# Kernel optimization log

Measured on AMD Instinct MI355X. Metric: run time of the kernel, lower is better.

Reference implementation:

```python
import jax, jax.numpy as jnp
import numpy as np
from jax import lax

B, T, F, H, L = 64, 2048, 128, 128, 2


def _lstm_layer(x, Wih, Whh, bih, bhh, h0, c0):
    """Single LSTM layer, torch gate order (i,f,g,o). x: [B,T,in] -> y: [B,T,H], hT, cT."""
    b = bih + bhh

    def step(carry, xt):
        h, c = carry
        gates = xt @ Wih.T + h @ Whh.T + b  # [B,4H]
        i, f, g, o = jnp.split(gates, 4, axis=-1)
        i = jax.nn.sigmoid(i)
        f = jax.nn.sigmoid(f)
        g = jnp.tanh(g)
        o = jax.nn.sigmoid(o)
        c = f * c + i * g
        h = o * jnp.tanh(c)
        return (h, c), h

    xs = jnp.swapaxes(x, 0, 1)  # [T,B,in]
    (hT, cT), ys = lax.scan(step, (h0, c0), xs)
    return jnp.swapaxes(ys, 0, 1), hT, cT


def setup_inputs() -> dict:
    key = jax.random.key(0)
    ks = jax.random.split(key, 20)
    s = 1.0 / np.sqrt(H)
    u = lambda k, shape: jax.random.uniform(k, shape, jnp.float32, -s, s)
    inp = {"x": jax.random.normal(ks[0], (B, T, F), jnp.float32)}
    i = 1
    for pre, in0 in (("enc", F), ("dec", H)):
        for l in range(L):
            d_in = in0 if l == 0 else H
            inp[f"{pre}_Wih{l}"] = u(ks[i], (4 * H, d_in)); i += 1
            inp[f"{pre}_Whh{l}"] = u(ks[i], (4 * H, H)); i += 1
            inp[f"{pre}_bih{l}"] = u(ks[i], (4 * H,)); i += 1
            inp[f"{pre}_bhh{l}"] = u(ks[i], (4 * H,)); i += 1
    inp["out_W"] = u(ks[i], (F, H)); i += 1
    inp["out_b"] = u(ks[i], (F,))
    return inp


def reference(x,
              enc_Wih0, enc_Whh0, enc_bih0, enc_bhh0,
              enc_Wih1, enc_Whh1, enc_bih1, enc_bhh1,
              dec_Wih0, dec_Whh0, dec_bih0, dec_bhh0,
              dec_Wih1, dec_Whh1, dec_bih1, dec_bhh1,
              out_W, out_b):
    z = jnp.zeros((x.shape[0], H), x.dtype)
    # encoder: 2 stacked layers, zero initial state
    y0, h0, c0 = _lstm_layer(x, enc_Wih0, enc_Whh0, enc_bih0, enc_bhh0, z, z)
    y1, h1, c1 = _lstm_layer(y0, enc_Wih1, enc_Whh1, enc_bih1, enc_bhh1, z, z)
    # decoder: zeros input, initial state = encoder final (h,c) per layer
    dec_in = jnp.zeros_like(x)  # valid since n_features == hidden_dim
    d0, _, _ = _lstm_layer(dec_in, dec_Wih0, dec_Whh0, dec_bih0, dec_bhh0, h0, c0)
    d1, _, _ = _lstm_layer(d0, dec_Wih1, dec_Whh1, dec_bih1, dec_bhh1, h1, c1)
    return d1 @ out_W.T + out_b
```

## Files before the change

### kernel.cpp

```cpp
#include <hip/hip_runtime.h>
#include <cstdint>
#include <cstddef>

typedef float    float4v __attribute__((ext_vector_type(4)));
typedef _Float16 f16x4   __attribute__((ext_vector_type(4)));
typedef _Float16 f16x8   __attribute__((ext_vector_type(8)));
typedef unsigned long long u64;

#define DI __device__ __forceinline__

static const int Bsz = 64, Tlen = 2048, Hd = 128, G4 = 512;
static const int Mrows = Bsz * Tlen;
static const int HSTR = 144;
static const int RING = 256;
static const int YSTR = 136;

DI float sigf_fast(float x) {
    float e = __builtin_amdgcn_exp2f(-1.442695041f * x);
    return __builtin_amdgcn_rcpf(1.f + e);
}
DI float tanhf_fast(float x) {
    float e = __builtin_amdgcn_exp2f(-2.885390082f * x);
    return 2.f * __builtin_amdgcn_rcpf(1.f + e) - 1.f;
}

DI void lds_barrier() {
    asm volatile("s_waitcnt lgkmcnt(0)\n\ts_barrier" ::: "memory");
}

DI void pin(f16x8& v) {
    float4v t = __builtin_bit_cast(float4v, v);
    asm volatile("" : "+v"(t));
    v = __builtin_bit_cast(f16x8, t);
}

DI f16x8 cvt8(const float* p) {
    float4v u = *(const float4v*)p;
    float4v w = *(const float4v*)(p + 4);
    f16x8 o;
    o[0] = (_Float16)u[0]; o[1] = (_Float16)u[1]; o[2] = (_Float16)u[2]; o[3] = (_Float16)u[3];
    o[4] = (_Float16)w[0]; o[5] = (_Float16)w[1]; o[6] = (_Float16)w[2]; o[7] = (_Float16)w[3];
    return o;
}

DI u64 ald64(const void* pp) {
    return __hip_atomic_load((const u64*)pp, __ATOMIC_RELAXED, __HIP_MEMORY_SCOPE_AGENT);
}
DI void ast16(void* pp, unsigned short v) {
    __hip_atomic_store((unsigned short*)pp, v, __ATOMIC_RELAXED, __HIP_MEMORY_SCOPE_AGENT);
}
DI unsigned int aldu32(const unsigned int* pp) {
    return __hip_atomic_load(pp, __ATOMIC_RELAXED, __HIP_MEMORY_SCOPE_AGENT);
}
DI void astu32(unsigned int* pp, unsigned int v) {
    __hip_atomic_store(pp, v, __ATOMIC_RELAXED, __HIP_MEMORY_SCOPE_AGENT);
}

template <bool A_F16, bool PERM, bool OUT_F32>
__global__ __launch_bounds__(256) void gemm_k128(
    const void* __restrict__ Av, const float* __restrict__ W,
    const float* __restrict__ bias, void* __restrict__ Cout, int M, int N)
{
    const int lane = threadIdx.x & 63, wave = threadIdx.x >> 6;
    const int m0 = blockIdx.y * 64 + wave * 16;
    const int n0 = blockIdx.x * 64;
    const int r15 = lane & 15, kg = lane >> 4;

    f16x8 a[4];
    if (A_F16) {
        const f16x8* Ar = (const f16x8*)((const _Float16*)Av + (size_t)(m0 + r15) * 128);
#pragma unroll
        for (int kt = 0; kt < 4; kt++) a[kt] = Ar[kt * 4 + kg];
    } else {
        const float* Ar = (const float*)Av + (size_t)(m0 + r15) * 128;
#pragma unroll
        for (int kt = 0; kt < 4; kt++) a[kt] = cvt8(Ar + kt * 32 + kg * 8);
    }

    f16x8 bfrg[4][4];
#pragma unroll
    for (int nt = 0; nt < 4; nt++) {
        int n = n0 + nt * 16 + r15;
        int wrow = PERM ? ((n & 3) * 128 + (n >> 2)) : n;
        const float* Wr = W + (size_t)wrow * 128;
#pragma unroll
        for (int kt = 0; kt < 4; kt++) bfrg[nt][kt] = cvt8(Wr + kt * 32 + kg * 8);
    }

    float4v acc[4] = {};
#pragma unroll
    for (int kt = 0; kt < 4; kt++)
#pragma unroll
        for (int nt = 0; nt < 4; nt++)
            acc[nt] = __builtin_amdgcn_mfma_f32_16x16x32_f16(a[kt], bfrg[nt][kt], acc[nt], 0, 0, 0);

#pragma unroll
    for (int nt = 0; nt < 4; nt++) {
        int n = n0 + nt * 16 + r15;
        float bv = bias ? bias[n] : 0.f;
#pragma unroll
        for (int r = 0; r < 4; r++) {
            int m = m0 + kg * 4 + r;
            float v = acc[nt][r] + bv;
            if (OUT_F32) ((float*)Cout)[(size_t)m * N + n] = v;
            else         ((_Float16*)Cout)[(size_t)m * N + n] = (_Float16)v;
        }
    }
}

template <bool P_HAS_XP, bool P_INIT, bool C_INIT, bool C_WRITE_Y>
__global__ __launch_bounds__(512, 1) void lstm_fused3(
    const float* __restrict__ Up, const float* __restrict__ bip, const float* __restrict__ bhp,
    const _Float16* __restrict__ XPp,
    const float* __restrict__ php, const float* __restrict__ pcp,
    float* __restrict__ fhp, float* __restrict__ fcp,
    const float* __restrict__ Wc, const float* __restrict__ Uc,
    const float* __restrict__ bic, const float* __restrict__ bhc,
    const float* __restrict__ phc, const float* __restrict__ pcc,
    float* __restrict__ fhc, float* __restrict__ fcc,
    _Float16* __restrict__ PB,
    _Float16* __restrict__ X2,
    _Float16* __restrict__ Yc,
    unsigned int* __restrict__ prog, unsigned int* __restrict__ prog2, int T)
{
    const int tid  = threadIdx.x;
    const int lane = tid & 63, w = tid >> 6;
    const int col  = lane & 15, quad = lane >> 4;
    const int b    = col & 3, s = col >> 2;
    const int role = blockIdx.x >> 4;
    const int p    = blockIdx.x & 15;
    const int bglob = p * 4 + b;
    const int j    = w * 16 + s * 4 + quad;
    const int NG   = T >> 3;

    __shared__ alignas(16) _Float16 Hl[2 * 4 * HSTR];
    __shared__ alignas(16) _Float16 Ylh[32 * YSTR];

    unsigned int* pr  = prog  + p * 16;
    unsigned int* pr2 = prog2 + p * 16;

    if (role == 0) {
        f16x8 af[4][4];
#pragma unroll
        for (int mt = 0; mt < 4; mt++) {
            int urow = (col & 3) * 128 + (w * 16 + mt * 4 + (col >> 2));
            const float* ur = Up + (size_t)urow * 128;
#pragma unroll
            for (int kc = 0; kc < 4; kc++) af[mt][kc] = cvt8(ur + kc * 32 + quad * 8);
        }
#pragma unroll
        for (int mt = 0; mt < 4; mt++)
#pragma unroll
            for (int kc = 0; kc < 4; kc++) pin(af[mt][kc]);

        float bq[4];
#pragma unroll
        for (int q = 0; q < 4; q++) bq[q] = bip[q * 128 + j] + bhp[q * 128 + j];

        float c = 0.f, hv = 0.f;
        if (P_INIT) {
            c  = pcp[(size_t)bglob * 128 + j];
            hv = php[(size_t)bglob * 128 + j];
        }
        Hl[b * HSTR + j] = (_Float16)hv;
        __syncthreads();

        const _Float16* xb = P_HAS_XP ? XPp + ((size_t)bglob * T) * 512 + 4 * j : nullptr;
        unsigned short* pbp = (unsigned short*)PB + (size_t)bglob * RING * 128 + j;
        f16x4 xp = {};
        if (P_HAS_XP) xp = *(const f16x4*)xb;

        int cur = 0;
        for (int g = 0; g < NG; g++) {
#pragma unroll
            for (int k = 0; k < 8; k++) {
                const int t = g * 8 + k;
                f16x4 xpn = {};
                if (P_HAS_XP) xpn = *(const f16x4*)(xb + (size_t)(t + 1) * 512);

                const _Float16* Hc = Hl + cur * (4 * HSTR);
                f16x8 bf[4];
#pragma unroll
                for (int kc = 0; kc < 4; kc++)
                    bf[kc] = *(const f16x8*)(Hc + b * HSTR + kc * 32 + quad * 8);

                float4v acc[4] = {};
#pragma unroll
                for (int kc = 0; kc < 4; kc++)
#pragma unroll
                    for (int mt = 0; mt < 4; mt++)
                        acc[mt] = __builtin_amdgcn_mfma_f32_16x16x32_f16(af[mt][kc], bf[kc], acc[mt], 0, 0, 0);

                float4v t0 = (s & 1) ? acc[1] : acc[0];
                float4v t1 = (s & 1) ? acc[3] : acc[2];
                float4v gg = (s & 2) ? t1 : t0;

                float g0 = gg[0] + bq[0], g1 = gg[1] + bq[1], g2 = gg[2] + bq[2], g3 = gg[3] + bq[3];
                if (P_HAS_XP) { g0 += (float)xp[0]; g1 += (float)xp[1]; g2 += (float)xp[2]; g3 += (float)xp[3]; }
                float iv = sigf_fast(g0), fv = sigf_fast(g1);
                float gv = tanhf_fast(g2), ov = sigf_fast(g3);
                c  = fv * c + iv * gv;
                hv = ov * tanhf_fast(c);

                _Float16 hf = (_Float16)hv;
                Hl[(cur ^ 1) * (4 * HSTR) + b * HSTR + j] = hf;

                ast16(pbp + (size_t)(t & (RING - 1)) * 128,
                      __builtin_bit_cast(unsigned short, hf));

                lds_barrier();
                xp = xpn;
                cur ^= 1;
            }
            if constexpr (P_HAS_XP) asm volatile("s_waitcnt vmcnt(2)" ::: "memory");
            else                    asm volatile("s_waitcnt vmcnt(1)" ::: "memory");
            if (tid == 0) astu32(pr, (unsigned int)(g * 8 + 7));
        }

        asm volatile("s_waitcnt vmcnt(0)" ::: "memory");
        __syncthreads();
        if (tid == 0) astu32(pr, (unsigned int)T);

        fhp[(size_t)bglob * 128 + j] = hv;
        fcp[(size_t)bglob * 128 + j] = c;
    } else if (role == 1) {
        f16x8 afH[4][4];
#pragma unroll
        for (int mt = 0; mt < 4; mt++) {
            int urow = (col & 3) * 128 + (w * 16 + mt * 4 + (col >> 2));
            const float* ur = Uc + (size_t)urow * 128;
#pragma unroll
            for (int kc = 0; kc < 4; kc++) afH[mt][kc] = cvt8(ur + kc * 32 + quad * 8);
        }
#pragma unroll
        for (int mt = 0; mt < 4; mt++)
#pragma unroll
            for (int kc = 0; kc < 4; kc++) pin(afH[mt][kc]);

        float bq[4];
#pragma unroll
        for (int q = 0; q < 4; q++) bq[q] = bic[q * 128 + j] + bhc[q * 128 + j];

        float c = 0.f, hv = 0.f;
        if (C_INIT) {
            c  = pcc[(size_t)bglob * 128 + j];
            hv = phc[(size_t)bglob * 128 + j];
        }
        Hl[b * HSTR + j] = (_Float16)hv;

        if (tid == 511) {
            unsigned int need = 9u; if (need > (unsigned int)T) need = (unsigned int)T;
            unsigned int psn = aldu32(pr2);
            while (psn < need) { __builtin_amdgcn_s_sleep(8); psn = aldu32(pr2); }
        }
        __syncthreads();

        const _Float16* x2b = X2 + (size_t)bglob * RING * 512 + 4 * j;
        f16x4 xp = __builtin_bit_cast(f16x4, ald64(x2b));

        int cur = 0;
        for (int g = 0; g < NG; g++) {
#pragma unroll
            for (int k = 0; k < 8; k++) {
                const int t = g * 8 + k;
                const int slot = (t + 1) & (RING - 1);
                f16x4 xpn = __builtin_bit_cast(f16x4, ald64(x2b + (size_t)slot * 512));

                const _Float16* Hc = Hl + cur * (4 * HSTR);
                f16x8 bf[4];
#pragma unroll
                for (int kc = 0; kc < 4; kc++)
                    bf[kc] = *(const f16x8*)(Hc + b * HSTR + kc * 32 + quad * 8);

                float4v acc[4] = {};
#pragma unroll
                for (int kc = 0; kc < 4; kc++)
#pragma unroll
                    for (int mt = 0; mt < 4; mt++)
                        acc[mt] = __builtin_amdgcn_mfma_f32_16x16x32_f16(afH[mt][kc], bf[kc], acc[mt], 0, 0, 0);

                float4v t0 = (s & 1) ? acc[1] : acc[0];
                float4v t1 = (s & 1) ? acc[3] : acc[2];
                float4v gg = (s & 2) ? t1 : t0;

                float g0 = gg[0] + bq[0] + (float)xp[0], g1 = gg[1] + bq[1] + (float)xp[1];
                float g2 = gg[2] + bq[2] + (float)xp[2], g3 = gg[3] + bq[3] + (float)xp[3];
                float iv = sigf_fast(g0), fv = sigf_fast(g1);
                float gv = tanhf_fast(g2), ov = sigf_fast(g3);
                c  = fv * c + iv * gv;
                hv = ov * tanhf_fast(c);

                _Float16 hf = (_Float16)hv;
                Hl[(cur ^ 1) * (4 * HSTR) + b * HSTR + j] = hf;
                if (C_WRITE_Y)
                    Yc[((size_t)bglob * T + t) * 128 + j] = hf;

                lds_barrier();
                xp = xpn;
                cur ^= 1;
            }
            if (tid == 511 && g + 1 < NG) {
                unsigned int need = (unsigned int)(8 * (g + 1) + 9);
                if (need > (unsigned int)T) need = (unsigned int)T;
                unsigned int psn = aldu32(pr2);
                while (psn < need) { __builtin_amdgcn_s_sleep(2); psn = aldu32(pr2); }
            }
            lds_barrier();
        }

        fhc[(size_t)bglob * 128 + j] = hv;
        fcc[(size_t)bglob * 128 + j] = c;
    } else {
        f16x8 bw[4][4];
#pragma unroll
        for (int nt = 0; nt < 4; nt++) {
            int n = (w * 4 + nt) * 16 + col;
            int wrow = (n & 3) * 128 + (n >> 2);
            const float* Wr = Wc + (size_t)wrow * 128;
#pragma unroll
            for (int kc = 0; kc < 4; kc++) bw[nt][kc] = cvt8(Wr + kc * 32 + quad * 8);
        }
#pragma unroll
        for (int nt = 0; nt < 4; nt++)
#pragma unroll
            for (int kc = 0; kc < 4; kc++) pin(bw[nt][kc]);

        const int lrow = tid >> 4, lchunk = tid & 15;
        const int lb = lrow & 3, ltr = lrow >> 2;

        for (int g = 0; g < NG; g++) {
            if (tid == 0) {
                unsigned int need = (unsigned int)(g * 8 + 8);
                unsigned int psn = aldu32(pr);
                while (psn < need) { __builtin_amdgcn_s_sleep(4); psn = aldu32(pr); }
            }
            __syncthreads();
            {
                int slot = (g * 8 + ltr) & (RING - 1);
                const char* srcp = (const char*)(PB + ((size_t)(p * 4 + lb) * RING + slot) * 128 + lchunk * 8);
                u64 a0 = ald64(srcp);
                u64 a1 = ald64(srcp + 8);
                char* dst = (char*)&Ylh[lrow * YSTR + lchunk * 8];
                *(u64*)dst = a0;
                *(u64*)(dst + 8) = a1;
            }
            lds_barrier();

            float4v acc[2][4] = {};
#pragma unroll
            for (int kc = 0; kc < 4; kc++) {
                f16x8 a0 = *(const f16x8*)&Ylh[col * YSTR + kc * 32 + quad * 8];
                f16x8 a1 = *(const f16x8*)&Ylh[(16 + col) * YSTR + kc * 32 + quad * 8];
#pragma unroll
                for (int nt = 0; nt < 4; nt++) {
                    acc[0][nt] = __builtin_amdgcn_mfma_f32_16x16x32_f16(a0, bw[nt][kc], acc[0][nt], 0, 0, 0);
                    acc[1][nt] = __builtin_amdgcn_mfma_f32_16x16x32_f16(a1, bw[nt][kc], acc[1][nt], 0, 0, 0);
                }
            }

#pragma unroll
            for (int mt = 0; mt < 2; mt++)
#pragma unroll
                for (int nt = 0; nt < 4; nt++) {
                    int n = (w * 4 + nt) * 16 + col;
#pragma unroll
                    for (int r = 0; r < 4; r++) {
                        int m = mt * 16 + quad * 4 + r;
                        int bb = m & 3, trow = m >> 2;
                        int slot = (g * 8 + trow) & (RING - 1);
                        _Float16 hval = (_Float16)acc[mt][nt][r];
                        ast16(X2 + ((size_t)(p * 4 + bb) * RING + slot) * 512 + n,
                              __builtin_bit_cast(unsigned short, hval));
                    }
                }

            asm volatile("s_waitcnt vmcnt(0)" ::: "memory");
            __syncthreads();
            if (tid == 0) astu32(pr2, (unsigned int)(g * 8 + 8));
        }
    }
}

extern "C" void kernel_launch(void* const* d_in, const int* in_sizes, int n_in,
                              void* d_out, int out_size, void* d_ws, size_t ws_size,
                              hipStream_t stream)
{
    const float* x    = (const float*)d_in[0];
    const float* eW0  = (const float*)d_in[1];
    const float* eU0  = (const float*)d_in[2];
    const float* eb0i = (const float*)d_in[3];
    const float* eb0h = (const float*)d_in[4];
    const float* eW1  = (const float*)d_in[5];
    const float* eU1  = (const float*)d_in[6];
    const float* eb1i = (const float*)d_in[7];
    const float* eb1h = (const float*)d_in[8];
    const float* dU0  = (const float*)d_in[10];
    const float* db0i = (const float*)d_in[11];
    const float* db0h = (const float*)d_in[12];
    const float* dW1  = (const float*)d_in[13];
    const float* dU1  = (const float*)d_in[14];
    const float* db1i = (const float*)d_in[15];
    const float* db1h = (const float*)d_in[16];
    const float* oW   = (const float*)d_in[17];
    const float* ob   = (const float*)d_in[18];

    char* ws = (char*)d_ws;
    _Float16* XP   = (_Float16*)ws;
    _Float16* Y    = (_Float16*)(ws + 134217728);
    _Float16* PB_A = (_Float16*)(ws + 134217728);
    _Float16* X2_A = (_Float16*)(ws + 134217728 + 4194304);
    _Float16* PB_B = (_Float16*)ws;
    _Float16* X2_B = (_Float16*)(ws + 4194304);
    float*    fh0 = (float*)(ws + 167772160);
    float*    fc0 = fh0 + Bsz * Hd;
    float*    fh1 = fc0 + Bsz * Hd;
    float*    fc1 = fh1 + Bsz * Hd;

    unsigned int* progA  = (unsigned int*)d_out;
    unsigned int* prog2A = progA + 16 * 16;
    unsigned int* progB  = progA + 32 * 16;
    unsigned int* prog2B = progA + 48 * 16;

    dim3 blk(256);
    dim3 gXP(G4 / 64, Mrows / 64);
    dim3 gOut(Hd / 64, Mrows / 64);

    hipMemsetAsync(d_out, 0, 4096, stream);

    gemm_k128<false, true, false><<<gXP, blk, 0, stream>>>((const void*)x, eW0, (const float*)nullptr, (void*)XP, Mrows, G4);

    lstm_fused3<true, false, false, false><<<dim3(48), dim3(512), 0, stream>>>(
        eU0, eb0i, eb0h, XP, (const float*)nullptr, (const float*)nullptr, fh0, fc0,
        eW1, eU1, eb1i, eb1h, (const float*)nullptr, (const float*)nullptr, fh1, fc1,
        PB_A, X2_A, (_Float16*)nullptr, progA, prog2A, Tlen);

    lstm_fused3<false, true, true, true><<<dim3(48), dim3(512), 0, stream>>>(
        dU0, db0i, db0h, (const _Float16*)nullptr, fh0, fc0, fh0, fc0,
        dW1, dU1, db1i, db1h, fh1, fc1, fh1, fc1,
        PB_B, X2_B, Y, progB, prog2B, Tlen);

    gemm_k128<true, false, true><<<gOut, blk, 0, stream>>>((const void*)Y, oW, ob, d_out, Mrows, Hd);
}
```

Before: 2.708 ms.

## Fuse input projection and output GEMM into persistent LSTM kernels as producer roles

```diff
diff --git a/kernel.cpp b/kernel.cpp
--- a/kernel.cpp
+++ b/kernel.cpp
@@ -6,11 +6,11 @@
 typedef _Float16 f16x4   __attribute__((ext_vector_type(4)));
 typedef _Float16 f16x8   __attribute__((ext_vector_type(8)));
 typedef unsigned long long u64;
+struct u64p { u64 a, b; };
 
 #define DI __device__ __forceinline__
 
 static const int Bsz = 64, Tlen = 2048, Hd = 128, G4 = 512;
-static const int Mrows = Bsz * Tlen;
 static const int HSTR = 144;
 static const int RING = 256;
 static const int YSTR = 136;
@@ -56,72 +56,24 @@
     __hip_atomic_store(pp, v, __ATOMIC_RELAXED, __HIP_MEMORY_SCOPE_AGENT);
 }
 
-template <bool A_F16, bool PERM, bool OUT_F32>
-__global__ __launch_bounds__(256) void gemm_k128(
-    const void* __restrict__ Av, const float* __restrict__ W,
-    const float* __restrict__ bias, void* __restrict__ Cout, int M, int N)
-{
-    const int lane = threadIdx.x & 63, wave = threadIdx.x >> 6;
-    const int m0 = blockIdx.y * 64 + wave * 16;
-    const int n0 = blockIdx.x * 64;
-    const int r15 = lane & 15, kg = lane >> 4;
-
-    f16x8 a[4];
-    if (A_F16) {
-        const f16x8* Ar = (const f16x8*)((const _Float16*)Av + (size_t)(m0 + r15) * 128);
-#pragma unroll
-        for (int kt = 0; kt < 4; kt++) a[kt] = Ar[kt * 4 + kg];
-    } else {
-        const float* Ar = (const float*)Av + (size_t)(m0 + r15) * 128;
-#pragma unroll
-        for (int kt = 0; kt < 4; kt++) a[kt] = cvt8(Ar + kt * 32 + kg * 8);
-    }
-
-    f16x8 bfrg[4][4];
-#pragma unroll
-    for (int nt = 0; nt < 4; nt++) {
-        int n = n0 + nt * 16 + r15;
-        int wrow = PERM ? ((n & 3) * 128 + (n >> 2)) : n;
-        const float* Wr = W + (size_t)wrow * 128;
-#pragma unroll
-        for (int kt = 0; kt < 4; kt++) bfrg[nt][kt] = cvt8(Wr + kt * 32 + kg * 8);
-    }
-
-    float4v acc[4] = {};
-#pragma unroll
-    for (int kt = 0; kt < 4; kt++)
-#pragma unroll
-        for (int nt = 0; nt < 4; nt++)
-            acc[nt] = __builtin_amdgcn_mfma_f32_16x16x32_f16(a[kt], bfrg[nt][kt], acc[nt], 0, 0, 0);
-
-#pragma unroll
-    for (int nt = 0; nt < 4; nt++) {
-        int n = n0 + nt * 16 + r15;
-        float bv = bias ? bias[n] : 0.f;
-#pragma unroll
-        for (int r = 0; r < 4; r++) {
-            int m = m0 + kg * 4 + r;
-            float v = acc[nt][r] + bv;
-            if (OUT_F32) ((float*)Cout)[(size_t)m * N + n] = v;
-            else         ((_Float16*)Cout)[(size_t)m * N + n] = (_Float16)v;
-        }
-    }
-}
-
-template <bool P_HAS_XP, bool P_INIT, bool C_INIT, bool C_WRITE_Y>
-__global__ __launch_bounds__(512, 1) void lstm_fused3(
+template <bool P_HAS_XP, bool P_INIT, bool C_INIT, bool R3_OUT>
+__global__ __launch_bounds__(512, 1) void lstm_fused4(
     const float* __restrict__ Up, const float* __restrict__ bip, const float* __restrict__ bhp,
-    const _Float16* __restrict__ XPp,
     const float* __restrict__ php, const float* __restrict__ pcp,
     float* __restrict__ fhp, float* __restrict__ fcp,
     const float* __restrict__ Wc, const float* __restrict__ Uc,
     const float* __restrict__ bic, const float* __restrict__ bhc,
     const float* __restrict__ phc, const float* __restrict__ pcc,
     float* __restrict__ fhc, float* __restrict__ fcc,
+    const float* __restrict__ Wx, const float* __restrict__ xin,
+    const float* __restrict__ oW, const float* __restrict__ ob,
+    float* __restrict__ outp,
     _Float16* __restrict__ PB,
     _Float16* __restrict__ X2,
-    _Float16* __restrict__ Yc,
-    unsigned int* __restrict__ prog, unsigned int* __restrict__ prog2, int T)
+    _Float16* __restrict__ X1,
+    _Float16* __restrict__ Y1,
+    unsigned int* __restrict__ prog,  unsigned int* __restrict__ prog2,
+    unsigned int* __restrict__ prog3, unsigned int* __restrict__ prog4, int T)
 {
     const int tid  = threadIdx.x;
     const int lane = tid & 63, w = tid >> 6;
@@ -138,6 +90,8 @@
 
     unsigned int* pr  = prog  + p * 16;
     unsigned int* pr2 = prog2 + p * 16;
+    unsigned int* pr3 = P_HAS_XP ? prog3 + p * 16 : nullptr;
+    unsigned int* pr4 = R3_OUT   ? prog4 + p * 16 : nullptr;
 
     if (role == 0) {
         f16x8 af[4][4];
@@ -165,10 +119,19 @@
         Hl[b * HSTR + j] = (_Float16)hv;
         __syncthreads();
 
-        const _Float16* xb = P_HAS_XP ? XPp + ((size_t)bglob * T) * 512 + 4 * j : nullptr;
+        const _Float16* x1b = P_HAS_XP ? X1 + (size_t)bglob * RING * 512 + 4 * j : nullptr;
         unsigned short* pbp = (unsigned short*)PB + (size_t)bglob * RING * 128 + j;
+
+        if constexpr (P_HAS_XP) {
+            if (tid == 511) {
+                unsigned int need = 16u; if (need > (unsigned int)T) need = (unsigned int)T;
+                unsigned int psn = aldu32(pr3);
+                while (psn < need) { __builtin_amdgcn_s_sleep(8); psn = aldu32(pr3); }
+            }
+            __syncthreads();
+        }
         f16x4 xp = {};
-        if (P_HAS_XP) xp = *(const f16x4*)xb;
+        if (P_HAS_XP) xp = __builtin_bit_cast(f16x4, ald64(x1b));
 
         int cur = 0;
         for (int g = 0; g < NG; g++) {
@@ -176,7 +139,8 @@
             for (int k = 0; k < 8; k++) {
                 const int t = g * 8 + k;
                 f16x4 xpn = {};
-                if (P_HAS_XP) xpn = *(const f16x4*)(xb + (size_t)(t + 1) * 512);
+                if (P_HAS_XP)
+                    xpn = __builtin_bit_cast(f16x4, ald64(x1b + (size_t)((t + 1) & (RING - 1)) * 512));
 
                 const _Float16* Hc = Hl + cur * (4 * HSTR);
                 f16x8 bf[4];
@@ -204,7 +168,6 @@
 
                 _Float16 hf = (_Float16)hv;
                 Hl[(cur ^ 1) * (4 * HSTR) + b * HSTR + j] = hf;
-
                 ast16(pbp + (size_t)(t & (RING - 1)) * 128,
                       __builtin_bit_cast(unsigned short, hf));
 
@@ -215,6 +178,15 @@
             if constexpr (P_HAS_XP) asm volatile("s_waitcnt vmcnt(2)" ::: "memory");
             else                    asm volatile("s_waitcnt vmcnt(1)" ::: "memory");
             if (tid == 0) astu32(pr, (unsigned int)(g * 8 + 7));
+            if constexpr (P_HAS_XP) {
+                if (tid == 511 && g + 1 < NG) {
+                    unsigned int need = (unsigned int)(8 * (g + 1) + 16);
+                    if (need > (unsigned int)T) need = (unsigned int)T;
+                    unsigned int psn = aldu32(pr3);
+                    while (psn < need) { __builtin_amdgcn_s_sleep(2); psn = aldu32(pr3); }
+                }
+                lds_barrier();
+            }
         }
 
         asm volatile("s_waitcnt vmcnt(0)" ::: "memory");
@@ -256,6 +228,7 @@
         __syncthreads();
 
         const _Float16* x2b = X2 + (size_t)bglob * RING * 512 + 4 * j;
+        unsigned short* y1p = R3_OUT ? (unsigned short*)Y1 + (size_t)bglob * T * 128 + j : nullptr;
         f16x4 xp = __builtin_bit_cast(f16x4, ald64(x2b));
 
         int cur = 0;
@@ -292,12 +265,16 @@
 
                 _Float16 hf = (_Float16)hv;
                 Hl[(cur ^ 1) * (4 * HSTR) + b * HSTR + j] = hf;
-                if (C_WRITE_Y)
-                    Yc[((size_t)bglob * T + t) * 128 + j] = hf;
+                if constexpr (R3_OUT)
+                    ast16(y1p + (size_t)t * 128, __builtin_bit_cast(unsigned short, hf));
 
                 lds_barrier();
                 xp = xpn;
                 cur ^= 1;
+            }
+            if constexpr (R3_OUT) {
+                asm volatile("s_waitcnt vmcnt(2)" ::: "memory");
+                if (tid == 0) astu32(pr4, (unsigned int)(g * 8 + 7));
             }
             if (tid == 511 && g + 1 < NG) {
                 unsigned int need = (unsigned int)(8 * (g + 1) + 9);
@@ -308,9 +285,14 @@
             lds_barrier();
         }
 
+        if constexpr (R3_OUT) {
+            asm volatile("s_waitcnt vmcnt(0)" ::: "memory");
+            __syncthreads();
+            if (tid == 0) astu32(pr4, (unsigned int)T);
+        }
         fhc[(size_t)bglob * 128 + j] = hv;
         fcc[(size_t)bglob * 128 + j] = c;
-    } else {
+    } else if (role == 2) {
         f16x8 bw[4][4];
 #pragma unroll
         for (int nt = 0; nt < 4; nt++) {
@@ -357,7 +339,6 @@
                     acc[1][nt] = __builtin_amdgcn_mfma_f32_16x16x32_f16(a1, bw[nt][kc], acc[1][nt], 0, 0, 0);
                 }
             }
-
 #pragma unroll
             for (int mt = 0; mt < 2; mt++)
 #pragma unroll
@@ -373,10 +354,120 @@
                               __builtin_bit_cast(unsigned short, hval));
                     }
                 }
-
             asm volatile("s_waitcnt vmcnt(0)" ::: "memory");
             __syncthreads();
             if (tid == 0) astu32(pr2, (unsigned int)(g * 8 + 8));
+        }
+    } else if constexpr (!R3_OUT) {
+        f16x8 bw[4][4];
+#pragma unroll
+        for (int nt = 0; nt < 4; nt++) {
+            int n = (w * 4 + nt) * 16 + col;
+            int wrow = (n & 3) * 128 + (n >> 2);
+            const float* Wr = Wx + (size_t)wrow * 128;
+#pragma unroll
+            for (int kc = 0; kc < 4; kc++) bw[nt][kc] = cvt8(Wr + kc * 32 + quad * 8);
+        }
+#pragma unroll
+        for (int nt = 0; nt < 4; nt++)
+#pragma unroll
+            for (int kc = 0; kc < 4; kc++) pin(bw[nt][kc]);
+
+        const int lrow = tid >> 4, lchunk = tid & 15;
+        const int lb = lrow & 3, ltr = lrow >> 2;
+        const float* xsrc = xin + (size_t)(p * 4 + lb) * T * 128 + lchunk * 8;
+
+        for (int g = 0; g < NG; g++) {
+            if (g >= 32 && tid == 0) {
+                unsigned int need = (unsigned int)(8 * (g - 32));
+                unsigned int psn = aldu32(pr);
+                while (psn < need) { __builtin_amdgcn_s_sleep(4); psn = aldu32(pr); }
+            }
+            __syncthreads();
+            {
+                f16x8 xv = cvt8(xsrc + (size_t)(g * 8 + ltr) * 128);
+                u64p w2 = __builtin_bit_cast(u64p, xv);
+                char* dst = (char*)&Ylh[lrow * YSTR + lchunk * 8];
+                *(u64*)dst = w2.a;
+                *(u64*)(dst + 8) = w2.b;
+            }
+            lds_barrier();
+
+            float4v acc[2][4] = {};
+#pragma unroll
+            for (int kc = 0; kc < 4; kc++) {
+                f16x8 a0 = *(const f16x8*)&Ylh[col * YSTR + kc * 32 + quad * 8];
+                f16x8 a1 = *(const f16x8*)&Ylh[(16 + col) * YSTR + kc * 32 + quad * 8];
+#pragma unroll
+                for (int nt = 0; nt < 4; nt++) {
+                    acc[0][nt] = __builtin_amdgcn_mfma_f32_16x16x32_f16(a0, bw[nt][kc], acc[0][nt], 0, 0, 0);
+                    acc[1][nt] = __builtin_amdgcn_mfma_f32_16x16x32_f16(a1, bw[nt][kc], acc[1][nt], 0, 0, 0);
+                }
+            }
+#pragma unroll
+            for (int mt = 0; mt < 2; mt++)
+#pragma unroll
+                for (int nt = 0; nt < 4; nt++) {
+                    int n = (w * 4 + nt) * 16 + col;
+#pragma unroll
+                    for (int r = 0; r < 4; r++) {
+                        int m = mt * 16 + quad * 4 + r;
+                        int bb = m & 3, trow = m >> 2;
+                        int slot = (g * 8 + trow) & (RING - 1);
+                        _Float16 hval = (_Float16)acc[mt][nt][r];
+                        ast16(X1 + ((size_t)(p * 4 + bb) * RING + slot) * 512 + n,
+                              __builtin_bit_cast(unsigned short, hval));
+                    }
+                }
+            asm volatile("s_waitcnt vmcnt(0)" ::: "memory");
+            __syncthreads();
+            if (tid == 0) astu32(pr3, (unsigned int)(g * 8 + 8));
+        }
+    } else {
+        const int n = w * 16 + col;
+        f16x8 bo[4];
+#pragma unroll
+        for (int kc = 0; kc < 4; kc++) bo[kc] = cvt8(oW + (size_t)n * 128 + kc * 32 + quad * 8);
+#pragma unroll
+        for (int kc = 0; kc < 4; kc++) pin(bo[kc]);
+        const float bv = ob[n];
+
+        const int lrow = tid >> 4, lchunk = tid & 15;
+        const int lb = lrow & 3, ltr = lrow >> 2;
+
+        for (int g = 0; g < NG; g++) {
+            if (tid == 0) {
+                unsigned int need = (unsigned int)(g * 8 + 8);
+                unsigned int psn = aldu32(pr4);
+                while (psn < need) { __builtin_amdgcn_s_sleep(4); psn = aldu32(pr4); }
+            }
+            __syncthreads();
+            {
+                const char* srcp = (const char*)(Y1 + ((size_t)(p * 4 + lb) * T + g * 8 + ltr) * 128 + lchunk * 8);
+                u64 a0 = ald64(srcp);
+                u64 a1 = ald64(srcp + 8);
+                char* dst = (char*)&Ylh[lrow * YSTR + lchunk * 8];
+                *(u64*)dst = a0;
+                *(u64*)(dst + 8) = a1;
+            }
+            lds_barrier();
+
+            float4v acc[2] = {};
+#pragma unroll
+            for (int kc = 0; kc < 4; kc++) {
+                f16x8 a0 = *(const f16x8*)&Ylh[col * YSTR + kc * 32 + quad * 8];
+                f16x8 a1 = *(const f16x8*)&Ylh[(16 + col) * YSTR + kc * 32 + quad * 8];
+                acc[0] = __builtin_amdgcn_mfma_f32_16x16x32_f16(a0, bo[kc], acc[0], 0, 0, 0);
+                acc[1] = __builtin_amdgcn_mfma_f32_16x16x32_f16(a1, bo[kc], acc[1], 0, 0, 0);
+            }
+#pragma unroll
+            for (int mt = 0; mt < 2; mt++)
+#pragma unroll
+                for (int r = 0; r < 4; r++) {
+                    int m = mt * 16 + quad * 4 + r;
+                    int bb = m & 3, trow = m >> 2;
+                    outp[((size_t)(p * 4 + bb) * T + g * 8 + trow) * 128 + n] = acc[mt][r] + bv;
+                }
         }
     }
 }
@@ -405,39 +496,39 @@
     const float* ob   = (const float*)d_in[18];
 
     char* ws = (char*)d_ws;
-    _Float16* XP   = (_Float16*)ws;
-    _Float16* Y    = (_Float16*)(ws + 134217728);
-    _Float16* PB_A = (_Float16*)(ws + 134217728);
-    _Float16* X2_A = (_Float16*)(ws + 134217728 + 4194304);
-    _Float16* PB_B = (_Float16*)ws;
-    _Float16* X2_B = (_Float16*)(ws + 4194304);
-    float*    fh0 = (float*)(ws + 167772160);
+    _Float16* X1  = (_Float16*)(ws);
+    _Float16* X2A = (_Float16*)(ws + (16u << 20));
+    _Float16* PBA = (_Float16*)(ws + (32u << 20));
+    _Float16* X2B = (_Float16*)(ws + (36u << 20));
+    _Float16* PBB = (_Float16*)(ws + (52u << 20));
+    _Float16* Y1  = (_Float16*)(ws + (56u << 20));
+    float*    fh0 = (float*)(ws + (88u << 20));
     float*    fc0 = fh0 + Bsz * Hd;
     float*    fh1 = fc0 + Bsz * Hd;
     float*    fc1 = fh1 + Bsz * Hd;
-
-    unsigned int* progA  = (unsigned int*)d_out;
-    unsigned int* prog2A = progA + 16 * 16;
-    unsigned int* progB  = progA + 32 * 16;
-    unsigned int* prog2B = progA + 48 * 16;
-
-    dim3 blk(256);
-    dim3 gXP(G4 / 64, Mrows / 64);
-    dim3 gOut(Hd / 64, Mrows / 64);
-
-    hipMemsetAsync(d_out, 0, 4096, stream);
-
-    gemm_k128<false, true, false><<<gXP, blk, 0, stream>>>((const void*)x, eW0, (const float*)nullptr, (void*)XP, Mrows, G4);
-
-    lstm_fused3<true, false, false, false><<<dim3(48), dim3(512), 0, stream>>>(
-        eU0, eb0i, eb0h, XP, (const float*)nullptr, (const float*)nullptr, fh0, fc0,
+    unsigned int* pg = (unsigned int*)(ws + (88u << 20) + (1u << 17));
+    unsigned int* progA  = pg + 0 * 256;
+    unsigned int* prog2A = pg + 1 * 256;
+    unsigned int* prog3A = pg + 2 * 256;
+    unsigned int* progB  = pg + 3 * 256;
+    unsigned int* prog2B = pg + 4 * 256;
+    unsigned int* prog4B = pg + 5 * 256;
+
+    hipMemsetAsync((void*)pg, 0, 8192, stream);
+
+    lstm_fused4<true, false, false, false><<<dim3(64), dim3(512), 0, stream>>>(
+        eU0, eb0i, eb0h, (const float*)nullptr, (const float*)nullptr, fh0, fc0,
         eW1, eU1, eb1i, eb1h, (const float*)nullptr, (const float*)nullptr, fh1, fc1,
-        PB_A, X2_A, (_Float16*)nullptr, progA, prog2A, Tlen);
-
-    lstm_fused3<false, true, true, true><<<dim3(48), dim3(512), 0, stream>>>(
-        dU0, db0i, db0h, (const _Float16*)nullptr, fh0, fc0, fh0, fc0,
+        eW0, x,
+        (const float*)nullptr, (const float*)nullptr, (float*)nullptr,
+        PBA, X2A, X1, (_Float16*)nullptr,
+        progA, prog2A, prog3A, (unsigned int*)nullptr, Tlen);
+
+    lstm_fused4<false, true, true, true><<<dim3(64), dim3(512), 0, stream>>>(
+        dU0, db0i, db0h, fh0, fc0, fh0, fc0,
         dW1, dU1, db1i, db1h, fh1, fc1, fh1, fc1,
-        PB_B, X2_B, Y, progB, prog2B, Tlen);
-
-    gemm_k128<true, false, true><<<gOut, blk, 0, stream>>>((const void*)Y, oW, ob, d_out, Mrows, Hd);
-}
+        (const float*)nullptr, (const float*)nullptr,
+        oW, ob, (float*)d_out,
+        PBB, X2B, (_Float16*)nullptr, Y1,
+        progB, prog2B, (unsigned int*)nullptr, prog4B, Tlen);
+}
```

After: 2.674 ms. Within noise of the previous version (-1.3%).
